# Kernel optimization log

Hardware: AMD Instinct MI355X
Metric: run time of the kernel (lower is better)

Reference implementation:

```python
import jax, jax.numpy as jnp
import numpy as np

B, T, D, H = 4, 4096, 1024, 16
CAP = 0.5


def setup_inputs() -> dict:
    key = jax.random.key(0)
    ks = jax.random.split(key, 8)
    s = 0.02
    n = lambda k, shape: jax.random.normal(k, shape, dtype=jnp.float32) * s
    return {
        "x": jax.random.normal(ks[0], (B, T, D), dtype=jnp.float32),
        "w_router": n(ks[1], (D,)),
        "in_proj_w": n(ks[2], (3 * D, D)),
        "in_proj_b": jnp.zeros((3 * D,), jnp.float32),
        "out_proj_w": n(ks[3], (D, D)),
        "out_proj_b": jnp.zeros((D,), jnp.float32),
        "w1": n(ks[4], (4 * D, D)),
        "b1": jnp.zeros((4 * D,), jnp.float32),
        "w2": n(ks[5], (D, 4 * D)),
        "b2": jnp.zeros((D,), jnp.float32),
        "ln1_g": jnp.ones((D,), jnp.float32),
        "ln1_b": jnp.zeros((D,), jnp.float32),
        "ln2_g": jnp.ones((D,), jnp.float32),
        "ln2_b": jnp.zeros((D,), jnp.float32),
    }


def _ln(x, g, b, eps=1e-5):
    mu = jnp.mean(x, -1, keepdims=True)
    var = jnp.var(x, -1, keepdims=True)  # population variance, matches torch LayerNorm
    return (x - mu) * jax.lax.rsqrt(var + eps) * g + b


def reference(x, w_router, in_proj_w, in_proj_b, out_proj_w, out_proj_b,
              w1, b1, w2, b2, ln1_g, ln1_b, ln2_g, ln2_b):
    Bx, Tx, Dx = x.shape
    k = max(1, int(Tx * CAP))  # tokens routed through the block, same k for every batch row
    logits = x @ w_router  # (B,T) scalar router scores
    aux = jnp.mean(logits ** 2) * 0.01
    # top-k selection; sort indices ascending = boolean-mask gather order in torch
    idx = jnp.sort(jax.lax.top_k(logits, k)[1], axis=-1)  # (B,k)
    xs = jnp.take_along_axis(x, idx[:, :, None], axis=1)  # (B,k,D)

    h = _ln(xs, ln1_g, ln1_b)
    qkv = h @ in_proj_w.T + in_proj_b  # (B,k,3D)
    q, kk, v = jnp.split(qkv, 3, axis=-1)
    dh = Dx // H
    heads = lambda t: t.reshape(Bx, k, H, dh).transpose(0, 2, 1, 3)  # (B,H,k,dh)
    q, kk, v = heads(q), heads(kk), heads(v)
    scores = jnp.einsum('bhqd,bhkd->bhqk', q, kk) / jnp.sqrt(jnp.float32(dh))
    attn = jax.nn.softmax(scores, axis=-1)
    o = jnp.einsum('bhqk,bhkd->bhqd', attn, v).transpose(0, 2, 1, 3).reshape(Bx, k, Dx)
    o = o @ out_proj_w.T + out_proj_b
    xs = xs + o
    h2 = _ln(xs, ln2_g, ln2_b)
    ff = jax.nn.gelu(h2 @ w1.T + b1, approximate=False) @ w2.T + b2
    xs = xs + ff
    # scatter processed tokens back; unselected tokens pass through unchanged
    out = x.at[jnp.arange(Bx)[:, None], idx].set(xs)
    return out, aux
```

## Files before the change

kernel.cpp:

```cpp
#include <hip/hip_runtime.h>

#define B_    4
#define T_    4096
#define D_    1024
#define H_    16
#define DH_   64
#define KTOK  2048
#define MROWS (B_*KTOK)

typedef unsigned short u16;
typedef __attribute__((ext_vector_type(8))) short short8;
typedef __attribute__((ext_vector_type(4))) float f32x4;
typedef __attribute__((ext_vector_type(4))) unsigned int u32x4;
typedef __attribute__((ext_vector_type(2))) unsigned int u32x2;
typedef __attribute__((ext_vector_type(4))) unsigned short u16x4;

static __device__ __forceinline__ u16 f2bf(float f) {
  union { float f; unsigned int u; } a; a.f = f;
  unsigned int u = a.u;
  unsigned int r = (u + 0x7FFFu + ((u >> 16) & 1u)) >> 16;
  return (u16)r;
}

#if defined(__has_builtin)
#if __has_builtin(__builtin_amdgcn_exp2f)
#define EXP2F(x) __builtin_amdgcn_exp2f(x)
#endif
#endif
#ifndef EXP2F
#define EXP2F(x) exp2f(x)
#endif

static __device__ __forceinline__ float gelu_f(float v) {
  float x = fabsf(v) * 0.70710678118654752f;
  float t = __builtin_amdgcn_rcpf(1.0f + 0.3275911f * x);
  float p = t * (0.254829592f + t * (-0.284496736f + t * (1.421413741f +
            t * (-1.453152027f + t * 1.061405429f))));
  float e = EXP2F(-1.4426950408889634f * x * x);
  float er = 1.0f - p * e;
  er = (v < 0.0f) ? -er : er;
  return 0.5f * v * (1.0f + er);
}

static __device__ __forceinline__ unsigned int pkbf_t(float a, float b) {
  unsigned int ua = __builtin_bit_cast(unsigned int, a);
  unsigned int ub = __builtin_bit_cast(unsigned int, b);
  return __builtin_amdgcn_perm(ub, ua, 0x07060302u);
}

static __device__ __forceinline__ void gld_lds16(const u16* g, u16* l) {
  __builtin_amdgcn_global_load_lds((__attribute__((address_space(1))) void*)g,
                                   (__attribute__((address_space(3))) void*)l, 16, 0, 0);
}

#define WAITV(N) asm volatile("s_waitcnt vmcnt(" #N ")" ::: "memory")

__global__ void __launch_bounds__(256) router_kernel(const float* __restrict__ x,
    const float* __restrict__ wr, float* __restrict__ logits, float* __restrict__ auxacc)
{
  int tid = threadIdx.x; int lane = tid & 63, wave = tid >> 6;
  int row = blockIdx.x * 4 + wave;
  const float* xr = x + (size_t)row * D_;
  float dot = 0.f;
#pragma unroll
  for (int j = 0; j < 4; j++) {
    int c = j * 256 + lane * 4;
    f32x4 xv = *(const f32x4*)(xr + c);
    f32x4 wv = *(const f32x4*)(wr + c);
    dot += xv[0]*wv[0] + xv[1]*wv[1] + xv[2]*wv[2] + xv[3]*wv[3];
  }
#pragma unroll
  for (int d = 1; d < 64; d <<= 1) dot += __shfl_xor(dot, d);
  __shared__ float red[4];
  if (lane == 0) { logits[row] = dot; red[wave] = dot; }
  __syncthreads();
  if (tid == 0) {
    float a = red[0]*red[0] + red[1]*red[1] + red[2]*red[2] + red[3]*red[3];
    atomicAdd(auxacc, a);
  }
}

__global__ void __launch_bounds__(256) rankp_kernel(const float* __restrict__ logits,
    int* __restrict__ rnk)
{
  __shared__ float ll[256];
  const int b = blockIdx.y, ch = blockIdx.z;
  const int tid = threadIdx.x;
  const float* lg = logits + (size_t)b * T_;
  const int j0 = ch * 256;
  ll[tid] = lg[j0 + tid];
  __syncthreads();
  const int t = blockIdx.x * 256 + tid;
  const float my = lg[t];
  int rank = 0;
#pragma unroll 4
  for (int j = 0; j < 256; j += 4) {
    f32x4 lj = *(const f32x4*)&ll[j];
    int jg = j0 + j;
    rank += (lj[0] > my) || (lj[0] == my && (jg+0) < t);
    rank += (lj[1] > my) || (lj[1] == my && (jg+1) < t);
    rank += (lj[2] > my) || (lj[2] == my && (jg+2) < t);
    rank += (lj[3] > my) || (lj[3] == my && (jg+3) < t);
  }
  atomicAdd(&rnk[(size_t)b * T_ + t], rank);
}

__global__ void __launch_bounds__(256) lnpass_kernel(const float* __restrict__ x,
    const int* __restrict__ rnk, const float* __restrict__ g, const float* __restrict__ bb,
    float* __restrict__ xs_out, u16* __restrict__ hout, float* __restrict__ out,
    int* __restrict__ idx, const float* __restrict__ acc, float* __restrict__ auxout)
{
  int row = blockIdx.x;
  int tid = threadIdx.x;
  if (row == 0 && tid == 0) auxout[0] = acc[0] * (0.01f / (float)(B_ * T_));
  const float* srow = x + (size_t)row * D_;
  f32x4 v = *(const f32x4*)(srow + tid * 4);
  int r = rnk[row];
  if (r >= KTOK) {
    *(f32x4*)(out + (size_t)row * D_ + tid * 4) = v;
    return;
  }
  if (tid == 0) idx[(row >> 12) * KTOK + r] = row & (T_ - 1);
  size_t mrow = (size_t)(row >> 12) * KTOK + r;
  float s  = v[0] + v[1] + v[2] + v[3];
  float sq = v[0]*v[0] + v[1]*v[1] + v[2]*v[2] + v[3]*v[3];
#pragma unroll
  for (int d = 1; d < 64; d <<= 1) { s += __shfl_xor(s, d); sq += __shfl_xor(sq, d); }
  __shared__ float rs[4], rq[4];
  int lane = tid & 63, wave = tid >> 6;
  if (lane == 0) { rs[wave] = s; rq[wave] = sq; }
  __syncthreads();
  s  = rs[0] + rs[1] + rs[2] + rs[3];
  sq = rq[0] + rq[1] + rq[2] + rq[3];
  float mean = s * (1.0f / D_);
  float var  = sq * (1.0f / D_) - mean * mean;
  float rstd = rsqrtf(var + 1e-5f);
  f32x4 gg = *(const f32x4*)(g + tid * 4);
  f32x4 bv = *(const f32x4*)(bb + tid * 4);
  *(f32x4*)(xs_out + mrow * D_ + tid * 4) = v;
  u16x4 o;
#pragma unroll
  for (int j = 0; j < 4; j++) o[j] = f2bf((v[j] - mean) * rstd * gg[j] + bv[j]);
  *(u16x4*)(hout + mrow * D_ + tid * 4) = o;
}

__global__ void __launch_bounds__(256) ln2_kernel(const float* __restrict__ src,
    const float* __restrict__ g, const float* __restrict__ bb, u16* __restrict__ hout)
{
  int row = blockIdx.x;
  int tid = threadIdx.x;
  const float* srow = src + (size_t)row * D_;
  f32x4 v = *(const f32x4*)(srow + tid * 4);
  float s  = v[0] + v[1] + v[2] + v[3];
  float sq = v[0]*v[0] + v[1]*v[1] + v[2]*v[2] + v[3]*v[3];
#pragma unroll
  for (int d = 1; d < 64; d <<= 1) { s += __shfl_xor(s, d); sq += __shfl_xor(sq, d); }
  __shared__ float rs[4], rq[4];
  int lane = tid & 63, wave = tid >> 6;
  if (lane == 0) { rs[wave] = s; rq[wave] = sq; }
  __syncthreads();
  s  = rs[0] + rs[1] + rs[2] + rs[3];
  sq = rq[0] + rq[1] + rq[2] + rq[3];
  float mean = s * (1.0f / D_);
  float var  = sq * (1.0f / D_) - mean * mean;
  float rstd = rsqrtf(var + 1e-5f);
  f32x4 gg = *(const f32x4*)(g + tid * 4);
  f32x4 bv = *(const f32x4*)(bb + tid * 4);
  u16x4 o;
#pragma unroll
  for (int j = 0; j < 4; j++) o[j] = f2bf((v[j] - mean) * rstd * gg[j] + bv[j]);
  *(u16x4*)(hout + (size_t)row * D_ + tid * 4) = o;
}

__global__ void __launch_bounds__(256) f2bf_all(const float* __restrict__ s0, const float* __restrict__ s1,
    const float* __restrict__ s2, const float* __restrict__ s3,
    u16* __restrict__ d0, u16* __restrict__ d1, u16* __restrict__ d2, u16* __restrict__ d3)
{
  const size_t c0 = (size_t)3 * D_ * D_, c1 = (size_t)4 * D_ * D_, c2 = (size_t)8 * D_ * D_;
  size_t e = (size_t)blockIdx.x * 1024 + (size_t)threadIdx.x * 4;
  const float* s; u16* d; size_t off;
  if (e < c0)      { s = s0; d = d0; off = e; }
  else if (e < c1) { s = s1; d = d1; off = e - c0; }
  else if (e < c2) { s = s2; d = d2; off = e - c1; }
  else             { s = s3; d = d3; off = e - c2; }
  f32x4 v = *(const f32x4*)(s + off);
  u16x4 o; o[0]=f2bf(v[0]); o[1]=f2bf(v[1]); o[2]=f2bf(v[2]); o[3]=f2bf(v[3]);
  *(u16x4*)(d + off) = o;
}

template<int EPI>
__global__ void __launch_bounds__(256, 2) gemm_bt(
    const u16* __restrict__ A, const u16* __restrict__ W,
    const float* __restrict__ bias, float* __restrict__ xs,
    u16* __restrict__ Cb, float* __restrict__ outf,
    const int* __restrict__ idx, u16* __restrict__ vtb, int M, int N, int K)
{
  __shared__ u16 As[2][128 * 64];
  __shared__ u16 Ws[2][128 * 64];
  const int tid = threadIdx.x;
  const int lane = tid & 63, wave = tid >> 6;
  const int m16 = lane & 15, quad = (lane >> 4) & 3;

  const int gx = gridDim.x;
  const int id = blockIdx.y * gx + blockIdx.x;
  const int cpx = (gx * (int)gridDim.y) >> 3;
  const int tl = (id & 7) * cpx + (id >> 3);
  const int bx = tl % gx, by = tl / gx;

  const size_t arow0 = (size_t)by * 128;
  const size_t wrow0 = (size_t)bx * 128;

  const int trow = tid >> 3;
  const int tcc  = (tid ^ trow) & 7;
  auto stagepc = [&](const u16* g0, u16* l0) {
    gld_lds16(g0 + (size_t)trow * K + tcc * 8,        l0 + (size_t)(tid & ~63) * 8);
    gld_lds16(g0 + (size_t)(32 + trow) * K + tcc * 8, l0 + 2048 + (size_t)(tid & ~63) * 8);
  };
  auto stage_tile = [&](int u, int s) {
    size_t kn = (size_t)u * 64;
    stagepc(A + (arow0)      * K + kn, &As[s][0]);
    stagepc(A + (arow0 + 64) * K + kn, &As[s][64 * 64]);
    stagepc(W + (wrow0)      * K + kn, &Ws[s][0]);
    stagepc(W + (wrow0 + 64) * K + kn, &Ws[s][64 * 64]);
  };

  auto ldA = [&](short8 (&f)[2][2], const u16* h) {
#pragma unroll
    for (int mt = 0; mt < 2; mt++) {
      int rr = wave * 32 + mt * 16 + m16;
      int sw = rr & 7;
#pragma unroll
      for (int kk = 0; kk < 2; kk++)
        f[mt][kk] = *(const short8*)&h[rr * 64 + (((kk * 4 + quad) ^ sw) * 8)];
    }
  };
  auto ldB = [&](short8 (&f)[4][2], const u16* h, int half) {
#pragma unroll
    for (int nt = 0; nt < 4; nt++) {
      int rb = half * 64 + nt * 16 + m16;
      int sw = rb & 7;
#pragma unroll
      for (int kk = 0; kk < 2; kk++)
        f[nt][kk] = *(const short8*)&h[rb * 64 + (((kk * 4 + quad) ^ sw) * 8)];
    }
  };

  f32x4 acc[2][8];
#pragma unroll
  for (int mt = 0; mt < 2; mt++)
#pragma unroll
    for (int n = 0; n < 8; n++) acc[mt][n] = (f32x4)0.0f;

  stage_tile(0, 0);

  const int NT = K >> 6;
  short8 af[2][2], bf[4][2], bf2[4][2];

  for (int t = 0; t < NT; t++) {
    const int cur = t & 1;
    const bool last = (t == NT - 1);

    WAITV(2);
    __builtin_amdgcn_s_barrier();
    __builtin_amdgcn_sched_barrier(0);
    if (!last) stage_tile(t + 1, cur ^ 1);

    ldA(af, &As[cur][0]);
    ldB(bf, &Ws[cur][0], 0);
    __builtin_amdgcn_s_setprio(1);
#pragma unroll
    for (int mt = 0; mt < 2; mt++)
#pragma unroll
      for (int nt = 0; nt < 4; nt++)
#pragma unroll
        for (int kk = 0; kk < 2; kk++)
          acc[mt][nt] = __builtin_amdgcn_mfma_f32_16x16x32_bf16(af[mt][kk], bf[nt][kk], acc[mt][nt], 0, 0, 0);
    __builtin_amdgcn_s_setprio(0);

    if (last) { WAITV(0); } else { WAITV(8); }
    __builtin_amdgcn_s_barrier();
    __builtin_amdgcn_sched_barrier(0);

    ldB(bf2, &Ws[cur][0], 1);
    __builtin_amdgcn_s_setprio(1);
#pragma unroll
    for (int mt = 0; mt < 2; mt++)
#pragma unroll
      for (int nt = 0; nt < 4; nt++)
#pragma unroll
        for (int kk = 0; kk < 2; kk++)
          acc[mt][4 + nt] = __builtin_amdgcn_mfma_f32_16x16x32_bf16(af[mt][kk], bf2[nt][kk], acc[mt][4 + nt], 0, 0, 0);
    __builtin_amdgcn_s_setprio(0);
  }

#pragma unroll
  for (int half = 0; half < 2; half++) {
#pragma unroll
    for (int mt = 0; mt < 2; mt++) {
#pragma unroll
      for (int nt = 0; nt < 4; nt++) {
        f32x4 a = acc[mt][half * 4 + nt];
        size_t col = wrow0 + half * 64 + nt * 16 + m16;
        float bvv = bias[col];
        size_t rowb = arow0 + wave * 32 + mt * 16 + quad * 4;
        if (EPI == 0) {
          if ((int)col < 2 * D_) {
            float sc = ((int)col < D_) ? 0.18033688f : 1.0f;
#pragma unroll
            for (int r = 0; r < 4; r++)
              Cb[(rowb + r) * (size_t)N + col] = f2bf((a[r] + bvv) * sc);
          } else {
            int hdh = (int)col - 2 * D_;
            int bb2 = (int)(rowb >> 11);
            int tok = (int)(rowb & (KTOK - 1));
            u16x4 o;
#pragma unroll
            for (int r = 0; r < 4; r++) o[r] = f2bf(a[r] + bvv);
            *(u16x4*)&vtb[(((size_t)(bb2 * H_) + (hdh >> 6)) * 64 + (hdh & 63)) * KTOK + tok] = o;
          }
        } else if (EPI == 1) {
#pragma unroll
          for (int r = 0; r < 4; r++) {
            size_t o = (rowb + r) * (size_t)N + col;
            xs[o] = xs[o] + (a[r] + bvv);
          }
        } else {
#pragma unroll
          for (int r = 0; r < 4; r++) {
            size_t row = rowb + r;
            int b = (int)(row >> 11);
            int i = (int)(row & (KTOK - 1));
            int t = idx[b * KTOK + i];
            float vv = xs[row * (size_t)D_ + col] + (a[r] + bvv);
            outf[((size_t)b * T_ + t) * D_ + col] = vv;
          }
        }
      }
    }
  }
}

__global__ void __launch_bounds__(512, 1) gemm_ff1(
    const u16* __restrict__ A, const u16* __restrict__ W,
    const float* __restrict__ bias, u16* __restrict__ Cb, int M, int N, int K)
{
  __shared__ u16 Asm[2][2][128 * 64];
  __shared__ u16 Bsm[2][2][128 * 64];

  const int tid = threadIdx.x;
  const int lane = tid & 63;
  const int w = tid >> 6;
  const int m16 = lane & 15, quad = (lane >> 4) & 3;
  const int rowA = (w >> 2) * 64;
  const int rowB = (w & 3) * 32;

  const int gx = gridDim.x;
  const int id = blockIdx.y * gx + blockIdx.x;
  const int cpx = (gx * (int)gridDim.y) >> 3;
  const int tl = (id & 7) * cpx + (id >> 3);
  const int bx = tl % gx, by = tl / gx;

  const int arow0 = by * 256;
  const int wcol0 = bx * 256;

  const int th8 = tid >> 3;
  const int ccs = (tid ^ th8) & 7;
  auto stage = [&](const u16* g0, u16* l0) {
    gld_lds16(g0 + (size_t)th8 * K + ccs * 8,        l0 + (size_t)(tid & ~63) * 8);
    gld_lds16(g0 + (size_t)(64 + th8) * K + ccs * 8, l0 + 4096 + (size_t)(tid & ~63) * 8);
  };
  auto stage_tile = [&](int u, int s) {
    size_t kn = (size_t)u * 64;
    stage(A + (size_t)arow0 * K + kn,         &Asm[s][0][0]);
    stage(W + (size_t)wcol0 * K + kn,         &Bsm[s][0][0]);
    stage(A + (size_t)(arow0 + 128) * K + kn, &Asm[s][1][0]);
    stage(W + (size_t)(wcol0 + 128) * K + kn, &Bsm[s][1][0]);
  };

  auto ldA = [&](short8 (&f)[4][2], const u16* h) {
#pragma unroll
    for (int mt = 0; mt < 4; mt++) {
      int rr = rowA + mt * 16 + m16;
      int sw = rr & 7;
#pragma unroll
      for (int kk = 0; kk < 2; kk++)
        f[mt][kk] = *(const short8*)&h[rr * 64 + (((kk * 4 + quad) ^ sw) * 8)];
    }
  };
  auto ldB = [&](short8 (&f)[2][2], const u16* h) {
#pragma unroll
    for (int nt = 0; nt < 2; nt++) {
      int rb = rowB + nt * 16 + m16;
      int sw = rb & 7;
#pragma unroll
      for (int kk = 0; kk < 2; kk++)
        f[nt][kk] = *(const short8*)&h[rb * 64 + (((kk * 4 + quad) ^ sw) * 8)];
    }
  };

  f32x4 acc[4][4][2];
#pragma unroll
  for (int q = 0; q < 4; q++)
#pragma unroll
    for (int mt = 0; mt < 4; mt++)
#pragma unroll
      for (int nt = 0; nt < 2; nt++) acc[q][mt][nt] = (f32x4)0.0f;

#define MMQ(QD, FA, FB) do { \
  __builtin_amdgcn_s_setprio(1); \
  _Pragma("unroll") for (int mt = 0; mt < 4; mt++) \
  _Pragma("unroll") for (int nt = 0; nt < 2; nt++) \
  _Pragma("unroll") for (int kk = 0; kk < 2; kk++) \
    acc[QD][mt][nt] = __builtin_amdgcn_mfma_f32_16x16x32_bf16(FA[mt][kk], FB[nt][kk], acc[QD][mt][nt], 0, 0, 0); \
  __builtin_amdgcn_s_setprio(0); } while (0)

  stage_tile(0, 0);

  const int NT = K >> 6;
  short8 af[4][2], af2[4][2], bf[2][2], bf2[2][2];

  for (int t = 0; t < NT; t++) {
    const int cur = t & 1;
    const bool last = (t == NT - 1);

    WAITV(4);
    __builtin_amdgcn_s_barrier();
    __builtin_amdgcn_sched_barrier(0);
    if (!last) stage_tile(t + 1, cur ^ 1);

    ldA(af, &Asm[cur][0][0]);
    ldB(bf, &Bsm[cur][0][0]);
    MMQ(0, af, bf);

    if (last) { WAITV(0); } else { WAITV(8); }
    __builtin_amdgcn_s_barrier();
    __builtin_amdgcn_sched_barrier(0);

    ldB(bf2, &Bsm[cur][1][0]);
    MMQ(1, af, bf2);
    ldA(af2, &Asm[cur][1][0]);
    MMQ(2, af2, bf);
    MMQ(3, af2, bf2);
  }
#undef MMQ

#pragma unroll
  for (int qd = 0; qd < 4; qd++) {
    const int ha = qd >> 1, hb = qd & 1;
#pragma unroll
    for (int mt = 0; mt < 4; mt++) {
#pragma unroll
      for (int nt = 0; nt < 2; nt++) {
        f32x4 a = acc[qd][mt][nt];
        size_t col = (size_t)wcol0 + hb * 128 + (w & 3) * 32 + nt * 16 + m16;
        float bvv = bias[col];
        size_t rowb = (size_t)arow0 + ha * 128 + (w >> 2) * 64 + mt * 16 + quad * 4;
#pragma unroll
        for (int r = 0; r < 4; r++)
          Cb[(rowb + r) * (size_t)N + col] = f2bf(gelu_f(a[r] + bvv));
      }
    }
  }
}

#define PSTR 72
__global__ void __launch_bounds__(256, 3) attn_kernel(const u16* __restrict__ qkv,
                                                      const u16* __restrict__ vtb,
                                                      u16* __restrict__ obuf)
{
  __shared__ u16 Ks[2][64 * 64];
  __shared__ u16 Vs[2][64 * 64];
  __shared__ u16 Ps[4][2][16 * PSTR];

  const int tid = threadIdx.x;
  const int lane = tid & 63, wave = tid >> 6;
  const int m16 = lane & 15, quad = lane >> 4;
  const int bh = blockIdx.x;
  const int b = bh >> 4, h = bh & 15;
  const int q0 = blockIdx.y * 128 + wave * 32;

  const u16* base = qkv + ((size_t)b * KTOK) * (3 * D_) + h * DH_;
  const u16* vb   = vtb + (size_t)bh * 64 * KTOK;

  short8 qf[2][2];
#pragma unroll
  for (int qh = 0; qh < 2; qh++) {
    const u16* qrow = base + (size_t)(q0 + qh * 16 + m16) * (3 * D_);
    qf[qh][0] = *(const short8*)(qrow + quad * 8);
    qf[qh][1] = *(const short8*)(qrow + 32 + quad * 8);
  }

  f32x4 oacc[2][4];
#pragma unroll
  for (int qh = 0; qh < 2; qh++)
#pragma unroll
    for (int nt = 0; nt < 4; nt++) oacc[qh][nt] = (f32x4)0.0f;
  f32x4 lsum[2] = {(f32x4)0.0f, (f32x4)0.0f};

  auto stage_tile = [&](const u16* g0, size_t rstride, u16* lds) {
#pragma unroll
    for (int c = 0; c < 2; c++) {
      int g = c * 256 + tid;
      int key = g >> 3;
      int cc = (g ^ key) & 7;
      gld_lds16(g0 + (size_t)key * rstride + cc * 8,
                lds + (size_t)(c * 256 + (tid & ~63)) * 8);
    }
  };

  stage_tile(base + D_, 3 * D_, &Ks[0][0]);
  stage_tile(vb, KTOK, &Vs[0][0]);
  __syncthreads();

  int buf = 0;
  for (int tk = 0; tk < KTOK; tk += 64) {
    if (tk + 64 < KTOK) {
      stage_tile(base + (size_t)(tk + 64) * (3 * D_) + D_, 3 * D_, &Ks[buf ^ 1][0]);
      stage_tile(vb + (tk + 64), KTOK, &Vs[buf ^ 1][0]);
    }
    const u16* Kb = &Ks[buf][0];
    const u16* Vb = &Vs[buf][0];

    f32x4 sacc[2][4];
#pragma unroll
    for (int qh = 0; qh < 2; qh++)
#pragma unroll
      for (int nt = 0; nt < 4; nt++) sacc[qh][nt] = (f32x4)0.0f;
    __builtin_amdgcn_s_setprio(1);
#pragma unroll
    for (int nt = 0; nt < 4; nt++) {
      int row = nt * 16 + m16;
      int sw = row & 7;
      short8 kf0 = *(const short8*)&Kb[row * 64 + ((quad ^ sw) * 8)];
      short8 kf1 = *(const short8*)&Kb[row * 64 + (((4 + quad) ^ sw) * 8)];
#pragma unroll
      for (int qh = 0; qh < 2; qh++) {
        sacc[qh][nt] = __builtin_amdgcn_mfma_f32_16x16x32_bf16(kf0, qf[qh][0], sacc[qh][nt], 0, 0, 0);
        sacc[qh][nt] = __builtin_amdgcn_mfma_f32_16x16x32_bf16(kf1, qf[qh][1], sacc[qh][nt], 0, 0, 0);
      }
    }
    __builtin_amdgcn_s_setprio(0);

    short8 vf[4][2];
#pragma unroll
    for (int nt = 0; nt < 4; nt++) {
      int row = nt * 16 + m16;
      int sw = row & 7;
      vf[nt][0] = *(const short8*)&Vb[row * 64 + ((quad ^ sw) * 8)];
      vf[nt][1] = *(const short8*)&Vb[row * 64 + (((4 + quad) ^ sw) * 8)];
    }

#pragma unroll
    for (int qh = 0; qh < 2; qh++) {
#pragma unroll
      for (int nt = 0; nt < 4; nt++) {
        f32x4 p;
#pragma unroll
        for (int r = 0; r < 4; r++) p[r] = EXP2F(sacc[qh][nt][r]);
        lsum[qh] += p;
        u32x2 w2; w2[0] = pkbf_t(p[0], p[1]); w2[1] = pkbf_t(p[2], p[3]);
        *(u32x2*)&Ps[wave][qh][m16 * PSTR + nt * 16 + quad * 4] = w2;
      }
    }
    short8 pa[2][2];
#pragma unroll
    for (int qh = 0; qh < 2; qh++) {
      pa[qh][0] = *(const short8*)&Ps[wave][qh][m16 * PSTR + quad * 8];
      pa[qh][1] = *(const short8*)&Ps[wave][qh][m16 * PSTR + 32 + quad * 8];
    }
    __builtin_amdgcn_s_setprio(1);
#pragma unroll
    for (int qh = 0; qh < 2; qh++)
#pragma unroll
      for (int nt = 0; nt < 4; nt++) {
        oacc[qh][nt] = __builtin_amdgcn_mfma_f32_16x16x32_bf16(pa[qh][0], vf[nt][0], oacc[qh][nt], 0, 0, 0);
        oacc[qh][nt] = __builtin_amdgcn_mfma_f32_16x16x32_bf16(pa[qh][1], vf[nt][1], oacc[qh][nt], 0, 0, 0);
      }
    __builtin_amdgcn_s_setprio(0);

    __syncthreads();
    buf ^= 1;
  }

  float rl[2][4];
#pragma unroll
  for (int qh = 0; qh < 2; qh++) {
    float l = (lsum[qh][0] + lsum[qh][1]) + (lsum[qh][2] + lsum[qh][3]);
    l += __shfl_xor(l, 16);
    l += __shfl_xor(l, 32);
#pragma unroll
    for (int r = 0; r < 4; r++) {
      float lr = __shfl(l, (lane & 48) | (quad * 4 + r));
      rl[qh][r] = 1.0f / lr;
    }
  }

#pragma unroll
  for (int qh = 0; qh < 2; qh++)
#pragma unroll
    for (int nt = 0; nt < 4; nt++)
#pragma unroll
      for (int r = 0; r < 4; r++) {
        int qq = q0 + qh * 16 + quad * 4 + r;
        float v = oacc[qh][nt][r] * rl[qh][r];
        obuf[((size_t)b * KTOK + qq) * D_ + h * DH_ + nt * 16 + m16] = f2bf(v);
      }
}

extern "C" void kernel_launch(void* const* d_in, const int* in_sizes, int n_in,
                              void* d_out, int out_size, void* d_ws, size_t ws_size,
                              hipStream_t stream)
{
  (void)in_sizes; (void)n_in; (void)out_size; (void)ws_size;
  const float* x          = (const float*)d_in[0];
  const float* w_router   = (const float*)d_in[1];
  const float* in_proj_w  = (const float*)d_in[2];
  const float* in_proj_b  = (const float*)d_in[3];
  const float* out_proj_w = (const float*)d_in[4];
  const float* out_proj_b = (const float*)d_in[5];
  const float* w1         = (const float*)d_in[6];
  const float* b1         = (const float*)d_in[7];
  const float* w2         = (const float*)d_in[8];
  const float* b2         = (const float*)d_in[9];
  const float* ln1g       = (const float*)d_in[10];
  const float* ln1b       = (const float*)d_in[11];
  const float* ln2g       = (const float*)d_in[12];
  const float* ln2b       = (const float*)d_in[13];
  float* out = (float*)d_out;

  char* w = (char*)d_ws;
  auto alloc = [&](size_t bytes) -> char* {
    char* p = w; w += (bytes + 255) & ~(size_t)255; return p;
  };
  float* logits = (float*)alloc((size_t)B_ * T_ * 4);
  int*   rnk    = (int*)  alloc((size_t)B_ * T_ * 4);
  int*   idx    = (int*)  alloc((size_t)B_ * KTOK * 4);
  float* auxacc = (float*)alloc(256);
  u16* inpw  = (u16*)alloc((size_t)3 * D_ * D_ * 2);
  u16* outpw = (u16*)alloc((size_t)D_ * D_ * 2);
  u16* w1b   = (u16*)alloc((size_t)4 * D_ * D_ * 2);
  u16* w2b   = (u16*)alloc((size_t)4 * D_ * D_ * 2);
  float* xs  = (float*)alloc((size_t)MROWS * D_ * 4);
  u16* hbuf  = (u16*)alloc((size_t)MROWS * D_ * 2);
  char* region = alloc((size_t)MROWS * 4 * D_ * 2);
  u16* qkvb = (u16*)region;
  u16* obuf = (u16*)(region + (size_t)MROWS * 3 * D_ * 2);
  u16* ffb  = (u16*)region;
  u16* vtb  = (u16*)alloc((size_t)B_ * H_ * DH_ * KTOK * 2);

  (void)hipMemsetAsync(auxacc, 0, 4, stream);
  (void)hipMemsetAsync(rnk, 0, (size_t)B_ * T_ * 4, stream);

  router_kernel<<<B_ * T_ / 4, 256, 0, stream>>>(x, w_router, logits, auxacc);
  rankp_kernel<<<dim3(T_ / 256, B_, 16), 256, 0, stream>>>(logits, rnk);
  lnpass_kernel<<<B_ * T_, 256, 0, stream>>>(x, rnk, ln1g, ln1b, xs, hbuf, out,
                                             idx, auxacc, out + (size_t)B_ * T_ * D_);

  f2bf_all<<<12 * D_ * D_ / 1024, 256, 0, stream>>>(in_proj_w, out_proj_w, w1, w2,
                                                    inpw, outpw, w1b, w2b);

  gemm_bt<0><<<dim3(3 * D_ / 128, MROWS / 128), 256, 0, stream>>>(
      hbuf, inpw, in_proj_b, nullptr, qkvb, nullptr, nullptr, vtb, MROWS, 3 * D_, D_);
  attn_kernel<<<dim3(B_ * H_, KTOK / 128), 256, 0, stream>>>(qkvb, vtb, obuf);
  gemm_bt<1><<<dim3(D_ / 128, MROWS / 128), 256, 0, stream>>>(
      obuf, outpw, out_proj_b, xs, nullptr, nullptr, nullptr, nullptr, MROWS, D_, D_);
  ln2_kernel<<<MROWS, 256, 0, stream>>>(xs, ln2g, ln2b, hbuf);
  gemm_ff1<<<dim3(4 * D_ / 256, MROWS / 256), 512, 0, stream>>>(
      hbuf, w1b, b1, ffb, MROWS, 4 * D_, D_);
  gemm_bt<3><<<dim3(D_ / 128, MROWS / 128), 256, 0, stream>>>(
      ffb, w2b, b2, xs, nullptr, out, idx, nullptr, MROWS, D_, 4 * D_);
}
```

Baseline: 626.1 us.

## Widen attention blocks to 8 waves, compute row sums via MFMA, swizzle P tile

The attention kernel now runs 512 threads (8 waves) per block covering 256 queries, so each staged K/V tile is shared by twice as many waves and each thread issues a single staging load. The softmax denominator is accumulated by extra MFMAs against a vector of bf16 ones instead of per-lane VALU adds followed by a shuffle reduction. The padded P scratch layout is replaced with an XOR-swizzled unpadded one. This trades extra MFMA work and a lower launch-bounds occupancy target for fewer VALU ops, fewer shuffles and less global-to-LDS traffic.

```diff
diff --git a/kernel.cpp b/kernel.cpp
--- a/kernel.cpp
+++ b/kernel.cpp
@@ -463,21 +463,20 @@
   }
 }
 
-#define PSTR 72
-__global__ void __launch_bounds__(256, 3) attn_kernel(const u16* __restrict__ qkv,
+__global__ void __launch_bounds__(512, 4) attn_kernel(const u16* __restrict__ qkv,
                                                       const u16* __restrict__ vtb,
                                                       u16* __restrict__ obuf)
 {
   __shared__ u16 Ks[2][64 * 64];
   __shared__ u16 Vs[2][64 * 64];
-  __shared__ u16 Ps[4][2][16 * PSTR];
+  __shared__ u16 Ps[8][2][16 * 64];
 
   const int tid = threadIdx.x;
   const int lane = tid & 63, wave = tid >> 6;
   const int m16 = lane & 15, quad = lane >> 4;
   const int bh = blockIdx.x;
   const int b = bh >> 4, h = bh & 15;
-  const int q0 = blockIdx.y * 128 + wave * 32;
+  const int q0 = blockIdx.y * 256 + wave * 32;
 
   const u16* base = qkv + ((size_t)b * KTOK) * (3 * D_) + h * DH_;
   const u16* vb   = vtb + (size_t)bh * 64 * KTOK;
@@ -489,29 +488,28 @@
     qf[qh][0] = *(const short8*)(qrow + quad * 8);
     qf[qh][1] = *(const short8*)(qrow + 32 + quad * 8);
   }
+  short8 vone;
+#pragma unroll
+  for (int i = 0; i < 8; i++) vone[i] = (short)0x3F80;
 
   f32x4 oacc[2][4];
 #pragma unroll
   for (int qh = 0; qh < 2; qh++)
 #pragma unroll
     for (int nt = 0; nt < 4; nt++) oacc[qh][nt] = (f32x4)0.0f;
-  f32x4 lsum[2] = {(f32x4)0.0f, (f32x4)0.0f};
+  f32x4 lacc[2] = {(f32x4)0.0f, (f32x4)0.0f};
 
   auto stage_tile = [&](const u16* g0, size_t rstride, u16* lds) {
-#pragma unroll
-    for (int c = 0; c < 2; c++) {
-      int g = c * 256 + tid;
-      int key = g >> 3;
-      int cc = (g ^ key) & 7;
-      gld_lds16(g0 + (size_t)key * rstride + cc * 8,
-                lds + (size_t)(c * 256 + (tid & ~63)) * 8);
-    }
+    int key = tid >> 3;
+    int cc = (tid ^ key) & 7;
+    gld_lds16(g0 + (size_t)key * rstride + cc * 8, lds + (size_t)(tid & ~63) * 8);
   };
 
   stage_tile(base + D_, 3 * D_, &Ks[0][0]);
   stage_tile(vb, KTOK, &Vs[0][0]);
   __syncthreads();
 
+  const int sw = m16 & 7;
   int buf = 0;
   for (int tk = 0; tk < KTOK; tk += 64) {
     if (tk + 64 < KTOK) {
@@ -530,9 +528,9 @@
 #pragma unroll
     for (int nt = 0; nt < 4; nt++) {
       int row = nt * 16 + m16;
-      int sw = row & 7;
-      short8 kf0 = *(const short8*)&Kb[row * 64 + ((quad ^ sw) * 8)];
-      short8 kf1 = *(const short8*)&Kb[row * 64 + (((4 + quad) ^ sw) * 8)];
+      int ksw = row & 7;
+      short8 kf0 = *(const short8*)&Kb[row * 64 + ((quad ^ ksw) * 8)];
+      short8 kf1 = *(const short8*)&Kb[row * 64 + (((4 + quad) ^ ksw) * 8)];
 #pragma unroll
       for (int qh = 0; qh < 2; qh++) {
         sacc[qh][nt] = __builtin_amdgcn_mfma_f32_16x16x32_bf16(kf0, qf[qh][0], sacc[qh][nt], 0, 0, 0);
@@ -545,9 +543,9 @@
 #pragma unroll
     for (int nt = 0; nt < 4; nt++) {
       int row = nt * 16 + m16;
-      int sw = row & 7;
-      vf[nt][0] = *(const short8*)&Vb[row * 64 + ((quad ^ sw) * 8)];
-      vf[nt][1] = *(const short8*)&Vb[row * 64 + (((4 + quad) ^ sw) * 8)];
+      int vsw = row & 7;
+      vf[nt][0] = *(const short8*)&Vb[row * 64 + ((quad ^ vsw) * 8)];
+      vf[nt][1] = *(const short8*)&Vb[row * 64 + (((4 + quad) ^ vsw) * 8)];
     }
 
 #pragma unroll
@@ -557,54 +555,48 @@
         f32x4 p;
 #pragma unroll
         for (int r = 0; r < 4; r++) p[r] = EXP2F(sacc[qh][nt][r]);
-        lsum[qh] += p;
         u32x2 w2; w2[0] = pkbf_t(p[0], p[1]); w2[1] = pkbf_t(p[2], p[3]);
-        *(u32x2*)&Ps[wave][qh][m16 * PSTR + nt * 16 + quad * 4] = w2;
+        int c16 = 2 * nt + (quad >> 1);
+        *(u32x2*)&Ps[wave][qh][m16 * 64 + ((c16 ^ sw) * 8) + (quad & 1) * 4] = w2;
       }
     }
     short8 pa[2][2];
 #pragma unroll
     for (int qh = 0; qh < 2; qh++) {
-      pa[qh][0] = *(const short8*)&Ps[wave][qh][m16 * PSTR + quad * 8];
-      pa[qh][1] = *(const short8*)&Ps[wave][qh][m16 * PSTR + 32 + quad * 8];
+      pa[qh][0] = *(const short8*)&Ps[wave][qh][m16 * 64 + ((quad ^ sw) * 8)];
+      pa[qh][1] = *(const short8*)&Ps[wave][qh][m16 * 64 + (((4 + quad) ^ sw) * 8)];
     }
     __builtin_amdgcn_s_setprio(1);
 #pragma unroll
-    for (int qh = 0; qh < 2; qh++)
+    for (int qh = 0; qh < 2; qh++) {
 #pragma unroll
       for (int nt = 0; nt < 4; nt++) {
         oacc[qh][nt] = __builtin_amdgcn_mfma_f32_16x16x32_bf16(pa[qh][0], vf[nt][0], oacc[qh][nt], 0, 0, 0);
         oacc[qh][nt] = __builtin_amdgcn_mfma_f32_16x16x32_bf16(pa[qh][1], vf[nt][1], oacc[qh][nt], 0, 0, 0);
       }
+      lacc[qh] = __builtin_amdgcn_mfma_f32_16x16x32_bf16(pa[qh][0], vone, lacc[qh], 0, 0, 0);
+      lacc[qh] = __builtin_amdgcn_mfma_f32_16x16x32_bf16(pa[qh][1], vone, lacc[qh], 0, 0, 0);
+    }
     __builtin_amdgcn_s_setprio(0);
 
     __syncthreads();
     buf ^= 1;
   }
 
-  float rl[2][4];
 #pragma unroll
   for (int qh = 0; qh < 2; qh++) {
-    float l = (lsum[qh][0] + lsum[qh][1]) + (lsum[qh][2] + lsum[qh][3]);
-    l += __shfl_xor(l, 16);
-    l += __shfl_xor(l, 32);
-#pragma unroll
-    for (int r = 0; r < 4; r++) {
-      float lr = __shfl(l, (lane & 48) | (quad * 4 + r));
-      rl[qh][r] = 1.0f / lr;
-    }
-  }
-
-#pragma unroll
-  for (int qh = 0; qh < 2; qh++)
+    f32x4 rl;
+#pragma unroll
+    for (int r = 0; r < 4; r++) rl[r] = 1.0f / lacc[qh][r];
 #pragma unroll
     for (int nt = 0; nt < 4; nt++)
 #pragma unroll
       for (int r = 0; r < 4; r++) {
         int qq = q0 + qh * 16 + quad * 4 + r;
-        float v = oacc[qh][nt][r] * rl[qh][r];
+        float v = oacc[qh][nt][r] * rl[r];
         obuf[((size_t)b * KTOK + qq) * D_ + h * DH_ + nt * 16 + m16] = f2bf(v);
       }
+  }
 }
 
 extern "C" void kernel_launch(void* const* d_in, const int* in_sizes, int n_in,
@@ -661,7 +653,7 @@
 
   gemm_bt<0><<<dim3(3 * D_ / 128, MROWS / 128), 256, 0, stream>>>(
       hbuf, inpw, in_proj_b, nullptr, qkvb, nullptr, nullptr, vtb, MROWS, 3 * D_, D_);
-  attn_kernel<<<dim3(B_ * H_, KTOK / 128), 256, 0, stream>>>(qkvb, vtb, obuf);
+  attn_kernel<<<dim3(B_ * H_, KTOK / 256), 512, 0, stream>>>(qkvb, vtb, obuf);
   gemm_bt<1><<<dim3(D_ / 128, MROWS / 128), 256, 0, stream>>>(
       obuf, outpw, out_proj_b, xs, nullptr, nullptr, nullptr, nullptr, MROWS, D_, D_);
   ln2_kernel<<<MROWS, 256, 0, stream>>>(xs, ln2g, ln2b, hbuf);
```

New measurement: 639.4 us. 1.02x slower.
